# Optimization experiments

Measured on AMD Instinct MI355X. Metric: run time of the kernel, lower is better.

Reference implementation:

```python
import jax, jax.numpy as jnp
import numpy as np

B, G = 128, 20000
HID = 64
NUM_BINS = 10
LEAKY_SLOPE = 0.01  # torch nn.LeakyReLU default


def setup_inputs() -> dict:
    key = jax.random.key(0)
    k1, k2, k3, k4, k5, k6 = jax.random.split(key, 6)
    vals = jax.random.normal(k1, (B, G), dtype=jnp.float32)
    keep = jax.random.uniform(k2, (B, G)) < 0.1
    expr_value = jnp.where(keep, vals, 0.0)
    # MLP params: Linear(1 -> HID), Linear(HID -> NUM_BINS-1)
    W1 = jax.random.normal(k3, (1, HID), dtype=jnp.float32) * 0.5
    b1 = jax.random.normal(k4, (HID,), dtype=jnp.float32) * 0.1
    W2 = jax.random.normal(k5, (HID, NUM_BINS - 1), dtype=jnp.float32) * (1.0 / np.sqrt(HID))
    b2 = jax.random.normal(k6, (NUM_BINS - 1,), dtype=jnp.float32) * 0.1
    return {"expr_value": expr_value, "W1": W1, "b1": b1, "W2": W2, "b2": b2}


def reference(expr_value, W1, b1, W2, b2):
    # mask of nonzero expression positions (B, G)
    mask_expr = (expr_value != 0).astype(jnp.float32)
    # tiny MLP applied to every position (vectorized; zero positions masked out below)
    x = expr_value[..., None]                      # (B, G, 1)
    h = x * W1[0] + b1                             # (B, G, HID); Linear(1->HID)
    h = jnp.where(h >= 0, h, LEAKY_SLOPE * h)      # LeakyReLU
    logits = jnp.einsum('bgh,hk->bgk', h, W2) + b2 # (B, G, NUM_BINS-1)
    p = jax.nn.softmax(logits, axis=-1)            # softmax over bins 1..num_bins-1
    m = mask_expr[..., None]
    # bin 0 prob = 1 where expr==0 else 0; bins 1.. = softmax where expr!=0 else 0
    probs = jnp.concatenate([1.0 - m, p * m], axis=-1)  # (B, G, NUM_BINS)
    return probs, mask_expr
```

## Files before the change

### kernel.cpp

```cpp
#include <hip/hip_runtime.h>
#include <math.h>

#define HID 64
#define KB 9
#define NB 10
#define NTOT (128 * 20000)
#define EPT 2
#define BLOCK 256
#define LEAKY 0.01f
#define RSTRIDE 20
#define SENT 3.0e38f
#define LOG2E 1.44269504088896f

#define NBUK 2048
#define BLO (-6.0f)
#define BW (12.0f / 2048.0f)
#define BSCALE (2048.0f / 12.0f)

#define TAB_U32 (128 + 65 * RSTRIDE)
#define WS_U32 (TAB_U32 + NBUK / 4)
#define WS_BYTES (WS_U32 * 4)

typedef float v4f __attribute__((ext_vector_type(4)));

__global__ __launch_bounds__(64) void setup_kernel(
    const float* __restrict__ W1, const float* __restrict__ b1,
    const float* __restrict__ W2, const float* __restrict__ b2,
    float* __restrict__ ws)
{
    __shared__ float t_lds[HID], w_lds[HID], b_lds[HID], tsrt[HID];
    __shared__ float w2_lds[HID * KB];
    __shared__ float red[18 * 65];

    const int j = threadIdx.x;
    const int blk = blockIdx.x;
    const float w = W1[j], b = b1[j];
    const float t = (w != 0.0f) ? (-b / w) : -SENT;
    t_lds[j] = t; w_lds[j] = w; b_lds[j] = b;
    if (blk < 65) {
        #pragma unroll
        for (int q = j; q < HID * KB; q += 64) w2_lds[q] = W2[q];
    }
    __syncthreads();

    int rank = 0;
    for (int i = 0; i < HID; ++i) {
        float ti = t_lds[i];
        rank += (ti < t || (ti == t && i < j)) ? 1 : 0;
    }
    tsrt[rank] = t;
    __syncthreads();

    if (blk >= 65) {
        const int bb = (blk - 65) * 64 + j;
        const float edge = BLO + ((float)bb - 0.5f) * BW;
        int cnt = 0;
        for (int i = 0; i < HID; ++i) cnt += (tsrt[i] <= edge) ? 1 : 0;
        ((unsigned char*)(ws + TAB_U32))[bb] = (bb == 0) ? 0 : (unsigned char)cnt;
        return;
    }

    const int r = blk;
    float xm;
    if (r == 0)        xm = tsrt[0] - 1.0f;
    else if (r == HID) xm = tsrt[HID - 1] + 1.0f;
    else               xm = 0.5f * (tsrt[r - 1] + tsrt[r]);

    const float s = (fmaf(w, xm, b) >= 0.0f) ? 1.0f : LEAKY;
    #pragma unroll
    for (int k = 0; k < KB; ++k) {
        const float w2s = w2_lds[j * KB + k] * s;
        red[(2 * k) * 65 + j]     = w2s * w;
        red[(2 * k + 1) * 65 + j] = w2s * b;
    }
    __syncthreads();

    if (j < 18) {
        float acc = 0.0f;
        for (int i = 0; i < HID; ++i) acc += red[j * 65 + i];
        const int k = j >> 1;
        if (j & 1) ws[128 + r * RSTRIDE + KB + k] = (acc + b2[k]) * LOG2E;
        else       ws[128 + r * RSTRIDE + k]      = acc * LOG2E;
    }
    if (r == 0) { ws[j] = tsrt[j]; ws[64 + j] = SENT; }
}

__global__ __launch_bounds__(BLOCK) void main_kernel(
    const float* __restrict__ expr, const float* __restrict__ ws,
    float* __restrict__ out)
{
    __shared__ __align__(16) unsigned int sdata[WS_U32];
    __shared__ v4f so[BLOCK * 5];

    const int tid = threadIdx.x;
    #pragma unroll
    for (int t = tid; t < WS_U32 / 4; t += BLOCK)
        ((v4f*)sdata)[t] = ((const v4f*)ws)[t];
    __syncthreads();

    const float* ts  = (const float*)sdata;
    const float* tab = (const float*)sdata + 128;
    const unsigned char* buk = (const unsigned char*)(sdata + TAB_U32);

    const int i0 = (blockIdx.x * BLOCK + tid) * EPT;
    const float2 xv = *(const float2*)(expr + i0);
    float x[EPT] = {xv.x, xv.y};
    float o[EPT * NB];
    float msk[EPT];
    #pragma unroll
    for (int e = 0; e < EPT; ++e) {
        const float xe = x[e];
        const float fb = fminf(2047.0f, fmaxf(0.0f, (xe - BLO) * BSCALE));
        int idx = buk[(int)fb];
        while (ts[idx] <= xe) ++idx;
        const v4f* rowv = (const v4f*)(tab + idx * RSTRIDE);
        v4f r0 = rowv[0], r1 = rowv[1], r2 = rowv[2], r3 = rowv[3], r4 = rowv[4];
        const float A[KB] = {r0.x, r0.y, r0.z, r0.w, r1.x, r1.y, r1.z, r1.w, r2.x};
        const float C[KB] = {r2.y, r2.z, r2.w, r3.x, r3.y, r3.z, r3.w, r4.x, r4.y};
        float lg[KB];
        #pragma unroll
        for (int k = 0; k < KB; ++k) lg[k] = fmaf(A[k], xe, C[k]);
        float m = lg[0];
        #pragma unroll
        for (int k = 1; k < KB; ++k) m = fmaxf(m, lg[k]);
        float p[KB];
        float s = 0.0f;
        #pragma unroll
        for (int k = 0; k < KB; ++k) { p[k] = exp2f(lg[k] - m); s += p[k]; }
        const float rcp = __frcp_rn(s);
        const bool nz = (xe != 0.0f);
        msk[e] = nz ? 1.0f : 0.0f;
        o[e * NB] = nz ? 0.0f : 1.0f;
        #pragma unroll
        for (int k = 0; k < KB; ++k) o[e * NB + 1 + k] = nz ? p[k] * rcp : 0.0f;
    }

    *(float2*)(out + (size_t)NTOT * NB + i0) = make_float2(msk[0], msk[1]);

    #pragma unroll
    for (int q = 0; q < 5; ++q) so[tid * 5 + q] = ((const v4f*)o)[q];
    __syncthreads();
    float* gout = out + (size_t)blockIdx.x * (BLOCK * EPT * NB);
    #pragma unroll
    for (int q = 0; q < 5; ++q) {
        const int g = q * BLOCK + tid;
        ((v4f*)gout)[g] = so[g];
    }
}

__global__ __launch_bounds__(BLOCK) void fused_kernel(
    const float* __restrict__ expr,
    const float* __restrict__ W1, const float* __restrict__ b1,
    const float* __restrict__ W2, const float* __restrict__ b2,
    float* __restrict__ out)
{
    __shared__ float ts[128];
    __shared__ float tab[65 * RSTRIDE];
    __shared__ float st[HID], sw[HID], sb[HID], tsrt[HID];
    const int tid = threadIdx.x;
    if (tid < HID) {
        float w = W1[tid], b = b1[tid];
        st[tid] = (w != 0.0f) ? (-b / w) : -SENT;
        sw[tid] = w; sb[tid] = b;
    }
    __syncthreads();
    if (tid < HID) {
        float t = st[tid];
        int r = 0;
        for (int i = 0; i < HID; ++i) {
            float ti = st[i];
            r += (ti < t || (ti == t && i < tid)) ? 1 : 0;
        }
        tsrt[r] = t;
    }
    __syncthreads();
    if (tid < 128) ts[tid] = (tid < HID) ? tsrt[tid] : SENT;
    for (int item = tid; item < 65 * KB; item += BLOCK) {
        int r = item / KB, k = item - r * KB;
        float xm;
        if (r == 0)        xm = tsrt[0] - 1.0f;
        else if (r == HID) xm = tsrt[HID - 1] + 1.0f;
        else               xm = 0.5f * (tsrt[r - 1] + tsrt[r]);
        float A = 0.0f, C = b2[k];
        for (int j = 0; j < HID; ++j) {
            float w = sw[j], bb = sb[j];
            float s = (fmaf(w, xm, bb) >= 0.0f) ? 1.0f : LEAKY;
            float w2s = W2[j * KB + k] * s;
            A = fmaf(w2s, w, A);
            C = fmaf(w2s, bb, C);
        }
        tab[r * RSTRIDE + k] = A;
        tab[r * RSTRIDE + KB + k] = C;
    }
    __syncthreads();
    const int i0 = (blockIdx.x * BLOCK + tid) * EPT;
    const float2 xv = *(const float2*)(expr + i0);
    float x[EPT] = {xv.x, xv.y};
    float o[EPT * NB]; float msk[EPT];
    #pragma unroll
    for (int e = 0; e < EPT; ++e) {
        const float xe = x[e];
        int idx = 0;
        #pragma unroll
        for (int s = 64; s >= 1; s >>= 1) idx += (ts[idx + s - 1] <= xe) ? s : 0;
        const float* row = tab + idx * RSTRIDE;
        float lg[KB];
        #pragma unroll
        for (int k = 0; k < KB; ++k) lg[k] = fmaf(row[k], xe, row[KB + k]);
        float m = lg[0];
        #pragma unroll
        for (int k = 1; k < KB; ++k) m = fmaxf(m, lg[k]);
        float p[KB]; float s = 0.0f;
        #pragma unroll
        for (int k = 0; k < KB; ++k) { p[k] = __expf(lg[k] - m); s += p[k]; }
        const float rcp = __frcp_rn(s);
        const bool nz = (xe != 0.0f);
        msk[e] = nz ? 1.0f : 0.0f;
        o[e * NB] = nz ? 0.0f : 1.0f;
        #pragma unroll
        for (int k = 0; k < KB; ++k) o[e * NB + 1 + k] = nz ? p[k] * rcp : 0.0f;
    }
    float* dst = out + (size_t)i0 * NB;
    #pragma unroll
    for (int q = 0; q < EPT * NB / 4; ++q) ((float4*)dst)[q] = ((const float4*)o)[q];
    *(float2*)(out + (size_t)NTOT * NB + i0) = make_float2(msk[0], msk[1]);
}

extern "C" void kernel_launch(void* const* d_in, const int* in_sizes, int n_in,
                              void* d_out, int out_size, void* d_ws, size_t ws_size,
                              hipStream_t stream) {
    const float* expr = (const float*)d_in[0];
    const float* W1   = (const float*)d_in[1];
    const float* b1   = (const float*)d_in[2];
    const float* W2   = (const float*)d_in[3];
    const float* b2   = (const float*)d_in[4];
    float* out = (float*)d_out;
    const int nblocks = NTOT / (BLOCK * EPT);

    if (ws_size >= (size_t)WS_BYTES) {
        float* ws = (float*)d_ws;
        setup_kernel<<<65 + NBUK / 64, 64, 0, stream>>>(W1, b1, W2, b2, ws);
        main_kernel<<<nblocks, BLOCK, 0, stream>>>(expr, ws, out);
    } else {
        fused_kernel<<<nblocks, BLOCK, 0, stream>>>(expr, W1, b1, W2, b2, out);
    }
}
```

Baseline: 140.8 us.

## Compact nonzero elements per block and compute softmax only for them

The main kernel now handles 2048 elements per block. It writes the default output (bin0=1, others 0) for every element with coalesced vector stores, then builds a compacted list of nonzero positions using a wave prefix-scan. Only the listed nonzeros run the table lookup and softmax, and their results are scattered back as 8-byte stores that overwrite the defaults. This skips the transcendental work for zeros, which make up about 90% of inputs. The cost is scattered, partly uncoalesced writes that rewrite some output bytes a second time, plus the extra scan and synchronisation.

Result: faster. 135.6 us (-3.7%).

```diff
diff --git a/kernel.cpp b/kernel.cpp
--- a/kernel.cpp
+++ b/kernel.cpp
@@ -5,8 +5,9 @@
 #define KB 9
 #define NB 10
 #define NTOT (128 * 20000)
-#define EPT 2
 #define BLOCK 256
+#define EPB 2048
+#define FEPT 2
 #define LEAKY 0.01f
 #define RSTRIDE 20
 #define SENT 3.0e38f
@@ -14,7 +15,6 @@
 
 #define NBUK 2048
 #define BLO (-6.0f)
-#define BW (12.0f / 2048.0f)
 #define BSCALE (2048.0f / 12.0f)
 
 #define TAB_U32 (128 + 65 * RSTRIDE)
@@ -22,6 +22,7 @@
 #define WS_BYTES (WS_U32 * 4)
 
 typedef float v4f __attribute__((ext_vector_type(4)));
+typedef float v2f __attribute__((ext_vector_type(2)));
 
 __global__ __launch_bounds__(64) void setup_kernel(
     const float* __restrict__ W1, const float* __restrict__ b1,
@@ -53,7 +54,7 @@
 
     if (blk >= 65) {
         const int bb = (blk - 65) * 64 + j;
-        const float edge = BLO + ((float)bb - 0.5f) * BW;
+        const float edge = BLO + ((float)bb - 0.5f) * (1.0f / BSCALE);
         int cnt = 0;
         for (int i = 0; i < HID; ++i) cnt += (tsrt[i] <= edge) ? 1 : 0;
         ((unsigned char*)(ws + TAB_U32))[bb] = (bb == 0) ? 0 : (unsigned char)cnt;
@@ -90,31 +91,80 @@
     float* __restrict__ out)
 {
     __shared__ __align__(16) unsigned int sdata[WS_U32];
-    __shared__ v4f so[BLOCK * 5];
+    __shared__ float xs[EPB];
+    __shared__ unsigned short list[EPB];
+    __shared__ int swsum[4];
 
     const int tid = threadIdx.x;
+    const int lane = tid & 63, wv = tid >> 6;
+
     #pragma unroll
     for (int t = tid; t < WS_U32 / 4; t += BLOCK)
         ((v4f*)sdata)[t] = ((const v4f*)ws)[t];
+
+    const size_t e0 = (size_t)blockIdx.x * EPB;
+    const v4f xa = ((const v4f*)(expr + e0))[tid];
+    const v4f xb = ((const v4f*)(expr + e0))[BLOCK + tid];
+    ((v4f*)xs)[tid] = xa;
+    ((v4f*)xs)[BLOCK + tid] = xb;
+    const float xr[8] = {xa.x, xa.y, xa.z, xa.w, xb.x, xb.y, xb.z, xb.w};
+
+    int c = 0;
+    #pragma unroll
+    for (int j = 0; j < 8; ++j) c += (xr[j] != 0.0f) ? 1 : 0;
+
+    int incl = c;
+    #pragma unroll
+    for (int d = 1; d < 64; d <<= 1) {
+        int n = __shfl_up(incl, d, 64);
+        if (lane >= d) incl += n;
+    }
+    if (lane == 63) swsum[wv] = incl;
+    __syncthreads();
+
+    const int s0 = swsum[0], s1 = swsum[1], s2 = swsum[2], s3 = swsum[3];
+    const int total = s0 + s1 + s2 + s3;
+    int base = (incl - c) + (wv > 0 ? s0 : 0) + (wv > 1 ? s1 : 0) + (wv > 2 ? s2 : 0);
+
+    #pragma unroll
+    for (int j = 0; j < 8; ++j) {
+        if (xr[j] != 0.0f) {
+            const int eidx = (j < 4) ? (4 * tid + j) : (1024 + 4 * tid + (j - 4));
+            list[base++] = (unsigned short)eidx;
+        }
+    }
+
+    float* mout = out + (size_t)NTOT * NB + e0;
+    const v4f ma = {xr[0] != 0.f ? 1.f : 0.f, xr[1] != 0.f ? 1.f : 0.f,
+                    xr[2] != 0.f ? 1.f : 0.f, xr[3] != 0.f ? 1.f : 0.f};
+    const v4f mb = {xr[4] != 0.f ? 1.f : 0.f, xr[5] != 0.f ? 1.f : 0.f,
+                    xr[6] != 0.f ? 1.f : 0.f, xr[7] != 0.f ? 1.f : 0.f};
+    ((v4f*)mout)[tid] = ma;
+    ((v4f*)mout)[BLOCK + tid] = mb;
+
+    float* gout = out + e0 * NB;
+    #pragma unroll
+    for (int q = 0; q < 20; ++q) {
+        const int g = q * BLOCK + tid;
+        const int r5 = g % 5;
+        const v4f v = {r5 == 0 ? 1.0f : 0.0f, 0.0f, r5 == 2 ? 1.0f : 0.0f, 0.0f};
+        ((v4f*)gout)[g] = v;
+    }
+
     __syncthreads();
 
     const float* ts  = (const float*)sdata;
     const float* tab = (const float*)sdata + 128;
     const unsigned char* buk = (const unsigned char*)(sdata + TAB_U32);
 
-    const int i0 = (blockIdx.x * BLOCK + tid) * EPT;
-    const float2 xv = *(const float2*)(expr + i0);
-    float x[EPT] = {xv.x, xv.y};
-    float o[EPT * NB];
-    float msk[EPT];
-    #pragma unroll
-    for (int e = 0; e < EPT; ++e) {
-        const float xe = x[e];
+    for (int i = tid; i < total; i += BLOCK) {
+        const int e = list[i];
+        const float xe = xs[e];
         const float fb = fminf(2047.0f, fmaxf(0.0f, (xe - BLO) * BSCALE));
         int idx = buk[(int)fb];
         while (ts[idx] <= xe) ++idx;
         const v4f* rowv = (const v4f*)(tab + idx * RSTRIDE);
-        v4f r0 = rowv[0], r1 = rowv[1], r2 = rowv[2], r3 = rowv[3], r4 = rowv[4];
+        const v4f r0 = rowv[0], r1 = rowv[1], r2 = rowv[2], r3 = rowv[3], r4 = rowv[4];
         const float A[KB] = {r0.x, r0.y, r0.z, r0.w, r1.x, r1.y, r1.z, r1.w, r2.x};
         const float C[KB] = {r2.y, r2.z, r2.w, r3.x, r3.y, r3.z, r3.w, r4.x, r4.y};
         float lg[KB];
@@ -128,23 +178,12 @@
         #pragma unroll
         for (int k = 0; k < KB; ++k) { p[k] = exp2f(lg[k] - m); s += p[k]; }
         const float rcp = __frcp_rn(s);
-        const bool nz = (xe != 0.0f);
-        msk[e] = nz ? 1.0f : 0.0f;
-        o[e * NB] = nz ? 0.0f : 1.0f;
-        #pragma unroll
-        for (int k = 0; k < KB; ++k) o[e * NB + 1 + k] = nz ? p[k] * rcp : 0.0f;
-    }
-
-    *(float2*)(out + (size_t)NTOT * NB + i0) = make_float2(msk[0], msk[1]);
-
-    #pragma unroll
-    for (int q = 0; q < 5; ++q) so[tid * 5 + q] = ((const v4f*)o)[q];
-    __syncthreads();
-    float* gout = out + (size_t)blockIdx.x * (BLOCK * EPT * NB);
-    #pragma unroll
-    for (int q = 0; q < 5; ++q) {
-        const int g = q * BLOCK + tid;
-        ((v4f*)gout)[g] = so[g];
+        v2f* po = (v2f*)(gout + (size_t)e * NB);
+        po[0] = (v2f){0.0f,        p[0] * rcp};
+        po[1] = (v2f){p[1] * rcp,  p[2] * rcp};
+        po[2] = (v2f){p[3] * rcp,  p[4] * rcp};
+        po[3] = (v2f){p[5] * rcp,  p[6] * rcp};
+        po[4] = (v2f){p[7] * rcp,  p[8] * rcp};
     }
 }
 
@@ -193,12 +232,12 @@
         tab[r * RSTRIDE + KB + k] = C;
     }
     __syncthreads();
-    const int i0 = (blockIdx.x * BLOCK + tid) * EPT;
+    const int i0 = (blockIdx.x * BLOCK + tid) * FEPT;
     const float2 xv = *(const float2*)(expr + i0);
-    float x[EPT] = {xv.x, xv.y};
-    float o[EPT * NB]; float msk[EPT];
-    #pragma unroll
-    for (int e = 0; e < EPT; ++e) {
+    float x[FEPT] = {xv.x, xv.y};
+    float o[FEPT * NB]; float msk[FEPT];
+    #pragma unroll
+    for (int e = 0; e < FEPT; ++e) {
         const float xe = x[e];
         int idx = 0;
         #pragma unroll
@@ -222,7 +261,7 @@
     }
     float* dst = out + (size_t)i0 * NB;
     #pragma unroll
-    for (int q = 0; q < EPT * NB / 4; ++q) ((float4*)dst)[q] = ((const float4*)o)[q];
+    for (int q = 0; q < FEPT * NB / 4; ++q) ((float4*)dst)[q] = ((const float4*)o)[q];
     *(float2*)(out + (size_t)NTOT * NB + i0) = make_float2(msk[0], msk[1]);
 }
 
@@ -235,13 +274,12 @@
     const float* W2   = (const float*)d_in[3];
     const float* b2   = (const float*)d_in[4];
     float* out = (float*)d_out;
-    const int nblocks = NTOT / (BLOCK * EPT);
 
     if (ws_size >= (size_t)WS_BYTES) {
         float* ws = (float*)d_ws;
         setup_kernel<<<65 + NBUK / 64, 64, 0, stream>>>(W1, b1, W2, b2, ws);
-        main_kernel<<<nblocks, BLOCK, 0, stream>>>(expr, ws, out);
+        main_kernel<<<NTOT / EPB, BLOCK, 0, stream>>>(expr, ws, out);
     } else {
-        fused_kernel<<<nblocks, BLOCK, 0, stream>>>(expr, W1, b1, W2, b2, out);
-    }
-}
+        fused_kernel<<<NTOT / (BLOCK * FEPT), BLOCK, 0, stream>>>(expr, W1, b1, W2, b2, out);
+    }
+}
```

## Split into dense zero-fill pass and compacted sparse scatter of nonzeros

Applied to the files above, without the earlier changes.

The single main kernel becomes two. A streaming kernel writes the default zero-position output and the mask for every element, and uses a wave prefix-sum plus an atomic to compact the nonzero (index, value) pairs into a workspace list. A scatter kernel then evaluates the piecewise-linear MLP and softmax only for listed nonzeros and overwrites their output rows. This avoids softmax work on the roughly 90% zero entries, at the cost of a third launch, an 8-byte-per-element workspace requirement, atomics, and scattered partial-row writes that overwrite lines already written.

Result: slower. 241.0 us (+71.2%).

```diff
diff --git a/kernel.cpp b/kernel.cpp
--- a/kernel.cpp
+++ b/kernel.cpp
@@ -5,7 +5,6 @@
 #define KB 9
 #define NB 10
 #define NTOT (128 * 20000)
-#define EPT 2
 #define BLOCK 256
 #define LEAKY 0.01f
 #define RSTRIDE 20
@@ -14,14 +13,16 @@
 
 #define NBUK 2048
 #define BLO (-6.0f)
-#define BW (12.0f / 2048.0f)
 #define BSCALE (2048.0f / 12.0f)
 
 #define TAB_U32 (128 + 65 * RSTRIDE)
-#define WS_U32 (TAB_U32 + NBUK / 4)
-#define WS_BYTES (WS_U32 * 4)
+#define SD_U32 (TAB_U32 + NBUK / 4)
+#define CNT_U32 2048
+#define LIST_U32 2056
+#define WS_BYTES (LIST_U32 * 4 + (size_t)NTOT * 8)
 
 typedef float v4f __attribute__((ext_vector_type(4)));
+typedef float v2f __attribute__((ext_vector_type(2)));
 
 __global__ __launch_bounds__(64) void setup_kernel(
     const float* __restrict__ W1, const float* __restrict__ b1,
@@ -34,6 +35,7 @@
 
     const int j = threadIdx.x;
     const int blk = blockIdx.x;
+    if (blk == 0 && j == 0) ((unsigned*)ws)[CNT_U32] = 0;
     const float w = W1[j], b = b1[j];
     const float t = (w != 0.0f) ? (-b / w) : -SENT;
     t_lds[j] = t; w_lds[j] = w; b_lds[j] = b;
@@ -53,7 +55,7 @@
 
     if (blk >= 65) {
         const int bb = (blk - 65) * 64 + j;
-        const float edge = BLO + ((float)bb - 0.5f) * BW;
+        const float edge = BLO + ((float)bb - 0.5f) * (1.0f / BSCALE);
         int cnt = 0;
         for (int i = 0; i < HID; ++i) cnt += (tsrt[i] <= edge) ? 1 : 0;
         ((unsigned char*)(ws + TAB_U32))[bb] = (bb == 0) ? 0 : (unsigned char)cnt;
@@ -85,36 +87,80 @@
     if (r == 0) { ws[j] = tsrt[j]; ws[64 + j] = SENT; }
 }
 
-__global__ __launch_bounds__(BLOCK) void main_kernel(
-    const float* __restrict__ expr, const float* __restrict__ ws,
+__global__ __launch_bounds__(BLOCK) void stream_kernel(
+    const float* __restrict__ expr, float* __restrict__ ws,
     float* __restrict__ out)
 {
-    __shared__ __align__(16) unsigned int sdata[WS_U32];
-    __shared__ v4f so[BLOCK * 5];
-
+    const int t = blockIdx.x * BLOCK + threadIdx.x;
+    const int lane = threadIdx.x & 63;
+
+    v4f* gp = (v4f*)out + (size_t)t * 10;
+    #pragma unroll
+    for (int j = 0; j < 10; ++j) {
+        const int r5 = j % 5;
+        const v4f v = {r5 == 0 ? 1.0f : 0.0f, 0.0f, r5 == 2 ? 1.0f : 0.0f, 0.0f};
+        gp[j] = v;
+    }
+
+    const v4f xv = ((const v4f*)expr)[t];
+    const float xr[4] = {xv.x, xv.y, xv.z, xv.w};
+    const v4f mv = {xr[0] != 0.f ? 1.f : 0.f, xr[1] != 0.f ? 1.f : 0.f,
+                    xr[2] != 0.f ? 1.f : 0.f, xr[3] != 0.f ? 1.f : 0.f};
+    ((v4f*)(out + (size_t)NTOT * NB))[t] = mv;
+
+    int c = 0;
+    #pragma unroll
+    for (int j = 0; j < 4; ++j) c += (xr[j] != 0.0f) ? 1 : 0;
+    int incl = c;
+    #pragma unroll
+    for (int d = 1; d < 64; d <<= 1) {
+        int n = __shfl_up(incl, d, 64);
+        if (lane >= d) incl += n;
+    }
+    const int wtotal = __shfl(incl, 63, 64);
+    unsigned wbase = 0;
+    if (lane == 63 && wtotal > 0)
+        wbase = atomicAdd((unsigned*)ws + CNT_U32, (unsigned)wtotal);
+    wbase = __shfl((int)wbase, 63, 64);
+
+    unsigned long long* list = (unsigned long long*)(ws + LIST_U32);
+    int off = (int)wbase + (incl - c);
+    #pragma unroll
+    for (int j = 0; j < 4; ++j) {
+        if (xr[j] != 0.0f) {
+            const unsigned eidx = 4u * (unsigned)t + (unsigned)j;
+            list[off++] = ((unsigned long long)eidx << 32) | (unsigned long long)__float_as_uint(xr[j]);
+        }
+    }
+}
+
+__global__ __launch_bounds__(BLOCK) void scatter_kernel(
+    const float* __restrict__ ws, float* __restrict__ out)
+{
+    const unsigned count = ((const unsigned*)ws)[CNT_U32];
+    if ((unsigned)blockIdx.x * BLOCK >= count) return;
+
+    __shared__ __align__(16) unsigned int sdata[SD_U32];
     const int tid = threadIdx.x;
     #pragma unroll
-    for (int t = tid; t < WS_U32 / 4; t += BLOCK)
-        ((v4f*)sdata)[t] = ((const v4f*)ws)[t];
+    for (int q = tid; q < SD_U32 / 4; q += BLOCK)
+        ((v4f*)sdata)[q] = ((const v4f*)ws)[q];
     __syncthreads();
 
     const float* ts  = (const float*)sdata;
     const float* tab = (const float*)sdata + 128;
     const unsigned char* buk = (const unsigned char*)(sdata + TAB_U32);
-
-    const int i0 = (blockIdx.x * BLOCK + tid) * EPT;
-    const float2 xv = *(const float2*)(expr + i0);
-    float x[EPT] = {xv.x, xv.y};
-    float o[EPT * NB];
-    float msk[EPT];
-    #pragma unroll
-    for (int e = 0; e < EPT; ++e) {
-        const float xe = x[e];
+    const unsigned long long* list = (const unsigned long long*)(ws + LIST_U32);
+
+    for (unsigned i = blockIdx.x * BLOCK + tid; i < count; i += gridDim.x * BLOCK) {
+        const unsigned long long pk = list[i];
+        const unsigned e = (unsigned)(pk >> 32);
+        const float xe = __uint_as_float((unsigned)pk);
         const float fb = fminf(2047.0f, fmaxf(0.0f, (xe - BLO) * BSCALE));
         int idx = buk[(int)fb];
         while (ts[idx] <= xe) ++idx;
         const v4f* rowv = (const v4f*)(tab + idx * RSTRIDE);
-        v4f r0 = rowv[0], r1 = rowv[1], r2 = rowv[2], r3 = rowv[3], r4 = rowv[4];
+        const v4f r0 = rowv[0], r1 = rowv[1], r2 = rowv[2], r3 = rowv[3], r4 = rowv[4];
         const float A[KB] = {r0.x, r0.y, r0.z, r0.w, r1.x, r1.y, r1.z, r1.w, r2.x};
         const float C[KB] = {r2.y, r2.z, r2.w, r3.x, r3.y, r3.z, r3.w, r4.x, r4.y};
         float lg[KB];
@@ -128,23 +174,12 @@
         #pragma unroll
         for (int k = 0; k < KB; ++k) { p[k] = exp2f(lg[k] - m); s += p[k]; }
         const float rcp = __frcp_rn(s);
-        const bool nz = (xe != 0.0f);
-        msk[e] = nz ? 1.0f : 0.0f;
-        o[e * NB] = nz ? 0.0f : 1.0f;
-        #pragma unroll
-        for (int k = 0; k < KB; ++k) o[e * NB + 1 + k] = nz ? p[k] * rcp : 0.0f;
-    }
-
-    *(float2*)(out + (size_t)NTOT * NB + i0) = make_float2(msk[0], msk[1]);
-
-    #pragma unroll
-    for (int q = 0; q < 5; ++q) so[tid * 5 + q] = ((const v4f*)o)[q];
-    __syncthreads();
-    float* gout = out + (size_t)blockIdx.x * (BLOCK * EPT * NB);
-    #pragma unroll
-    for (int q = 0; q < 5; ++q) {
-        const int g = q * BLOCK + tid;
-        ((v4f*)gout)[g] = so[g];
+        v2f* po = (v2f*)(out + (size_t)e * NB);
+        po[0] = (v2f){0.0f,       p[0] * rcp};
+        po[1] = (v2f){p[1] * rcp, p[2] * rcp};
+        po[2] = (v2f){p[3] * rcp, p[4] * rcp};
+        po[3] = (v2f){p[5] * rcp, p[6] * rcp};
+        po[4] = (v2f){p[7] * rcp, p[8] * rcp};
     }
 }
 
@@ -193,12 +228,12 @@
         tab[r * RSTRIDE + KB + k] = C;
     }
     __syncthreads();
-    const int i0 = (blockIdx.x * BLOCK + tid) * EPT;
+    const int i0 = (blockIdx.x * BLOCK + tid) * 2;
     const float2 xv = *(const float2*)(expr + i0);
-    float x[EPT] = {xv.x, xv.y};
-    float o[EPT * NB]; float msk[EPT];
-    #pragma unroll
-    for (int e = 0; e < EPT; ++e) {
+    float x[2] = {xv.x, xv.y};
+    float o[2 * NB]; float msk[2];
+    #pragma unroll
+    for (int e = 0; e < 2; ++e) {
         const float xe = x[e];
         int idx = 0;
         #pragma unroll
@@ -222,7 +257,7 @@
     }
     float* dst = out + (size_t)i0 * NB;
     #pragma unroll
-    for (int q = 0; q < EPT * NB / 4; ++q) ((float4*)dst)[q] = ((const float4*)o)[q];
+    for (int q = 0; q < 5; ++q) ((float4*)dst)[q] = ((const float4*)o)[q];
     *(float2*)(out + (size_t)NTOT * NB + i0) = make_float2(msk[0], msk[1]);
 }
 
@@ -235,13 +270,13 @@
     const float* W2   = (const float*)d_in[3];
     const float* b2   = (const float*)d_in[4];
     float* out = (float*)d_out;
-    const int nblocks = NTOT / (BLOCK * EPT);
-
-    if (ws_size >= (size_t)WS_BYTES) {
+
+    if (ws_size >= WS_BYTES) {
         float* ws = (float*)d_ws;
         setup_kernel<<<65 + NBUK / 64, 64, 0, stream>>>(W1, b1, W2, b2, ws);
-        main_kernel<<<nblocks, BLOCK, 0, stream>>>(expr, ws, out);
+        stream_kernel<<<NTOT / (BLOCK * 4), BLOCK, 0, stream>>>(expr, ws, out);
+        scatter_kernel<<<2560, BLOCK, 0, stream>>>(ws, out);
     } else {
-        fused_kernel<<<nblocks, BLOCK, 0, stream>>>(expr, W1, b1, W2, b2, out);
-    }
-}
+        fused_kernel<<<NTOT / (BLOCK * 2), BLOCK, 0, stream>>>(expr, W1, b1, W2, b2, out);
+    }
+}
```
